# Performance work log

Hardware: AMD Instinct MI355X
Metric: run time of the kernel (lower is better)

## Reference

```python
import jax, jax.numpy as jnp
import numpy as np

E = 20    # number of residue types (rc.restypes)
NB = 2    # num_blocks per AngleHead
NA = 7    # num_angles
C_S = 384
C_H = 128
BS, L = 8, 2048


def setup_inputs() -> dict:
    key = jax.random.key(0)
    ks = jax.random.split(key, 16)
    sc = 0.02
    return {
        "s": jax.random.normal(ks[0], (BS, L, C_S), dtype=jnp.float32),
        "s_init": jax.random.normal(ks[1], (BS, L, C_S), dtype=jnp.float32),
        "aatype": jax.random.randint(ks[2], (BS, L), 0, E, dtype=jnp.int32),
        # stacked per-residue-type AngleHead params
        "Win": jax.random.normal(ks[3], (E, C_S, C_H), dtype=jnp.float32) * sc,
        "b_in": jax.random.normal(ks[4], (E, C_H), dtype=jnp.float32) * sc,
        "Winit": jax.random.normal(ks[5], (E, C_S, C_H), dtype=jnp.float32) * sc,
        "b_init2": jax.random.normal(ks[6], (E, C_H), dtype=jnp.float32) * sc,
        "Wb1": jax.random.normal(ks[7], (E, NB, C_H, C_H), dtype=jnp.float32) * sc,
        "bb1": jax.random.normal(ks[8], (E, NB, C_H), dtype=jnp.float32) * sc,
        "Wb2": jax.random.normal(ks[9], (E, NB, C_H, C_H), dtype=jnp.float32) * sc,
        "bb2": jax.random.normal(ks[10], (E, NB, C_H), dtype=jnp.float32) * sc,
        "Wout": jax.random.normal(ks[11], (E, C_H, NA * 2), dtype=jnp.float32) * sc,
        "b_out": jax.random.normal(ks[12], (E, NA * 2), dtype=jnp.float32) * sc,
    }


def reference(s, s_init, aatype, Win, b_in, Winit, b_init2, Wb1, bb1, Wb2, bb2, Wout, b_out):
    relu = jax.nn.relu
    bs, seq_len, c_s = s.shape
    N = bs * seq_len
    sf = s.reshape(N, c_s)          # [N, c_s]
    si = s_init.reshape(N, c_s)     # [N, c_s]

    # Dense dispatch: run every token through all E per-type heads, then
    # combine with the one-hot routing mask (math identical to the torch
    # gather/scatter loop over residue types).
    h = jnp.einsum('nd,edh->neh', relu(sf), Win) + b_in            # [N,E,H]
    h = h + jnp.einsum('nd,edh->neh', relu(si), Winit) + b_init2   # [N,E,H]

    for b in range(NB):  # ResidualBlock1d: s + W2 @ relu(W1 @ relu(s))
        a = jnp.einsum('neh,ehk->nek', relu(h), Wb1[:, b]) + bb1[:, b]
        a = jnp.einsum('nek,ekh->neh', relu(a), Wb2[:, b]) + bb2[:, b]
        h = h + a

    out = jnp.einsum('neh,eho->neo', relu(h), Wout) + b_out        # [N,E,2*NA]
    sel = jax.nn.one_hot(aatype.reshape(N), E, dtype=out.dtype)    # [N,E]
    ang = jnp.einsum('neo,ne->no', out, sel).reshape(bs, seq_len, NA, 2)

    # F.normalize(dim=-1): x / max(||x||, eps)
    nrm = jnp.maximum(jnp.linalg.norm(ang, axis=-1, keepdims=True), 1e-12)
    return ang / nrm
```

## Files before the change

kernel.cpp:

```cpp
#include <hip/hip_runtime.h>
#include <math.h>

#define E_TYPES 20
#define NBLK 2
#define NANG 7
#define CS 384
#define CH 128
#define N_TOK (8 * 2048)
#define TOK 32
#define TPB 256
#define KC 128
#define MAX_TILES (N_TOK / TOK + E_TYPES)
#define NPREP 64

#define HIST_OFF 0
#define CNT_OFF 1536
#define POFF_OFF 1600
#define PERM_OFF 2048

#define WT1_OFF (256 * 1024)
#define WT1_SZ  (20 * 8 * 24 * 2048)
#define WTR_OFF (WT1_OFF + WT1_SZ)

typedef __attribute__((ext_vector_type(8))) short bfrag;
typedef __attribute__((ext_vector_type(4))) float f32x4;

__device__ __forceinline__ void split_bf16(float x, unsigned short& h, unsigned short& l) {
    unsigned int u = __float_as_uint(x);
    unsigned int hb = (u + 0x7FFFu + ((u >> 16) & 1u)) & 0xFFFF0000u;
    h = (unsigned short)(hb >> 16);
    float r = x - __uint_as_float(hb);
    unsigned int v = __float_as_uint(r);
    l = (unsigned short)((v + 0x7FFFu + ((v >> 16) & 1u)) >> 16);
}

__global__ void prep1(const float* __restrict__ Win, const float* __restrict__ Winit,
                      const float* __restrict__ Wb1, const float* __restrict__ Wb2,
                      const int* __restrict__ aatype, int* __restrict__ wsI,
                      unsigned short* __restrict__ wt) {
    __shared__ int lh[E_TYPES];
    int bid = blockIdx.x;
    int t = threadIdx.x;
    if (bid >= 1600) {
        int b2 = bid - 1600;
        if (t < E_TYPES) lh[t] = 0;
        __syncthreads();
        int idx = b2 * 256 + t;
        if (idx < N_TOK) atomicAdd(&lh[aatype[idx]], 1);
        __syncthreads();
        if (t < E_TYPES) wsI[HIST_OFF + b2 * E_TYPES + t] = lh[t];
        return;
    }
    int gid = bid * 256 + t;
    unsigned short h[8], l[8];
    if (gid < 245760) {
        int lane = gid & 63;
        int bi = gid >> 6;
        int kb = bi % 24;
        int r = bi / 24;
        int nt = r & 7, e = r >> 3;
        int n = nt * 16 + (lane & 15);
        int k0 = kb * 32 + (lane >> 4) * 8;
        #pragma unroll
        for (int j = 0; j < 8; j++) {
            int k = k0 + j;
            float x = (k < CS) ? Win[((size_t)e * CS + k) * CH + n]
                               : Winit[((size_t)e * CS + (k - CS)) * CH + n];
            split_bf16(x, h[j], l[j]);
        }
        unsigned short* dst = wt + (WT1_OFF / 2) + (size_t)bi * 1024 + lane * 8;
        *(bfrag*)dst = *(bfrag*)h;
        *(bfrag*)(dst + 512) = *(bfrag*)l;
    } else {
        gid -= 245760;
        int lane = gid & 63;
        int bi = gid >> 6;
        int kb = bi & 3;
        int nt = (bi >> 2) & 7;
        int m4 = (bi >> 5) & 3;
        int e = bi >> 7;
        int b = m4 >> 1;
        const float* W = (m4 & 1) ? Wb2 : Wb1;
        int n = nt * 16 + (lane & 15);
        int k0 = kb * 32 + (lane >> 4) * 8;
        #pragma unroll
        for (int j = 0; j < 8; j++) {
            int k = k0 + j;
            float x = W[(((size_t)e * NBLK + b) * CH + k) * CH + n];
            split_bf16(x, h[j], l[j]);
        }
        unsigned short* dst = wt + (WTR_OFF / 2) + (size_t)bi * 1024 + lane * 8;
        *(bfrag*)dst = *(bfrag*)h;
        *(bfrag*)(dst + 512) = *(bfrag*)l;
    }
}

__global__ void scatter_k(const int* __restrict__ aatype, int* ws) {
    __shared__ int lhist[NPREP * E_TYPES];
    __shared__ int counts[E_TYPES], poff[E_TYPES + 1], mybase[E_TYPES], lcur[E_TYPES];
    int t = threadIdx.x;
    int bid = blockIdx.x;
    for (int idx = t; idx < NPREP * E_TYPES; idx += TPB)
        lhist[idx] = ws[HIST_OFF + idx];
    if (t < E_TYPES) lcur[t] = 0;
    __syncthreads();
    if (t < E_TYPES) {
        int tot = 0, pre = 0;
        for (int b = 0; b < NPREP; b++) {
            int v = lhist[b * E_TYPES + t];
            tot += v;
            if (b < bid) pre += v;
        }
        counts[t] = tot;
        mybase[t] = pre;
    }
    __syncthreads();
    if (t == 0) {
        int off = 0;
        for (int e = 0; e < E_TYPES; e++) {
            poff[e] = off;
            off += (counts[e] + TOK - 1) & ~(TOK - 1);
        }
        poff[E_TYPES] = off;
    }
    __syncthreads();
    if (t < E_TYPES) mybase[t] += poff[t];
    __syncthreads();
    int idx = bid * blockDim.x + t;
    if (idx < N_TOK) {
        int e = aatype[idx];
        int r = atomicAdd(&lcur[e], 1);
        ws[PERM_OFF + mybase[e] + r] = idx;
    }
    if (bid == 0) {
        if (t < E_TYPES) ws[CNT_OFF + t] = counts[t];
        if (t == 0)
            for (int e = 0; e <= E_TYPES; e++) ws[POFF_OFF + e] = poff[e];
    }
}

#define MFMA(a, b, c) __builtin_amdgcn_mfma_f32_16x16x32_bf16((a), (b), (c), 0, 0, 0)

__global__ __launch_bounds__(TPB)
void angle_main(const float* __restrict__ s, const float* __restrict__ si,
                const float* __restrict__ b_in, const float* __restrict__ b_init2,
                const float* __restrict__ bb1, const float* __restrict__ bb2,
                const float* __restrict__ Wout, const float* __restrict__ b_out,
                const int* __restrict__ wsI, const unsigned short* __restrict__ wt,
                float* __restrict__ out)
{
    __shared__ unsigned short Ah[TOK][136];
    __shared__ unsigned short Al[TOK][136];
    __shared__ float Hf[TOK][132];
    __shared__ float Of[TOK][16];
    __shared__ int ptok[TOK];

    int pos = blockIdx.x * TOK;
    if (pos >= wsI[POFF_OFF + E_TYPES]) return;
    int e = 0;
    while (e < E_TYPES - 1 && pos >= wsI[POFF_OFF + e + 1]) e++;
    int n = wsI[CNT_OFF + e] - (pos - wsI[POFF_OFF + e]);
    if (n > TOK) n = TOK;

    int t = threadIdx.x;
    if (t < TOK) ptok[t] = wsI[PERM_OFF + pos + ((t < n) ? t : 0)];

    int w = t >> 6, lane = t & 63;
    int lane15 = lane & 15, quad = lane >> 4;
    int nc[2] = { (2 * w) * 16 + lane15, (2 * w + 1) * 16 + lane15 };

    const bfrag* wt1 = (const bfrag*)((const char*)wt + WT1_OFF);
    const bfrag* wtr = (const bfrag*)((const char*)wt + WTR_OFF);

    f32x4 acc[2][2];
    {
        float bv0 = b_in[e * CH + nc[0]] + b_init2[e * CH + nc[0]];
        float bv1 = b_in[e * CH + nc[1]] + b_init2[e * CH + nc[1]];
        #pragma unroll
        for (int mt = 0; mt < 2; mt++) {
            acc[mt][0] = (f32x4){bv0, bv0, bv0, bv0};
            acc[mt][1] = (f32x4){bv1, bv1, bv1, bv1};
        }
    }

    __syncthreads();

    int srow = t >> 3;
    int scol = (t & 7) * 16;
    for (int c = 0; c < 6; c++) {
        const float* src = (c < 3) ? s : si;
        int kb0 = (c < 3 ? c : c - 3) * KC;
        {
            const float4* rp = (const float4*)(src + (size_t)ptok[srow] * CS + kb0 + scol);
            #pragma unroll
            for (int q = 0; q < 4; q++) {
                float4 v = rp[q];
                ushort4 hv, lv;
                split_bf16(fmaxf(v.x, 0.f), hv.x, lv.x);
                split_bf16(fmaxf(v.y, 0.f), hv.y, lv.y);
                split_bf16(fmaxf(v.z, 0.f), hv.z, lv.z);
                split_bf16(fmaxf(v.w, 0.f), hv.w, lv.w);
                *(ushort4*)&Ah[srow][scol + 4 * q] = hv;
                *(ushort4*)&Al[srow][scol + 4 * q] = lv;
            }
        }
        __syncthreads();
        #pragma unroll
        for (int ks = 0; ks < 4; ks++) {
            int kb = c * 4 + ks;
            int kl = ks * 32 + quad * 8;
            bfrag ah0 = *(const bfrag*)&Ah[lane15][kl];
            bfrag ah1 = *(const bfrag*)&Ah[16 + lane15][kl];
            bfrag al0 = *(const bfrag*)&Al[lane15][kl];
            bfrag al1 = *(const bfrag*)&Al[16 + lane15][kl];
            size_t b0 = ((size_t)(e * 8 + 2 * w) * 24 + kb) * 128;
            size_t b1 = ((size_t)(e * 8 + 2 * w + 1) * 24 + kb) * 128;
            bfrag bh0 = wt1[b0 + lane],      bl0 = wt1[b0 + 64 + lane];
            bfrag bh1 = wt1[b1 + lane],      bl1 = wt1[b1 + 64 + lane];
            acc[0][0] = MFMA(ah0, bh0, acc[0][0]);
            acc[0][0] = MFMA(ah0, bl0, acc[0][0]);
            acc[0][0] = MFMA(al0, bh0, acc[0][0]);
            acc[0][1] = MFMA(ah0, bh1, acc[0][1]);
            acc[0][1] = MFMA(ah0, bl1, acc[0][1]);
            acc[0][1] = MFMA(al0, bh1, acc[0][1]);
            acc[1][0] = MFMA(ah1, bh0, acc[1][0]);
            acc[1][0] = MFMA(ah1, bl0, acc[1][0]);
            acc[1][0] = MFMA(al1, bh0, acc[1][0]);
            acc[1][1] = MFMA(ah1, bh1, acc[1][1]);
            acc[1][1] = MFMA(ah1, bl1, acc[1][1]);
            acc[1][1] = MFMA(al1, bh1, acc[1][1]);
        }
        __syncthreads();
    }

    for (int b = 0; b < NBLK; b++) {
        #pragma unroll
        for (int mt = 0; mt < 2; mt++)
            #pragma unroll
            for (int nl = 0; nl < 2; nl++) {
                f32x4 v = acc[mt][nl];
                #pragma unroll
                for (int r = 0; r < 4; r++) {
                    int m = mt * 16 + quad * 4 + r;
                    unsigned short hh, ll;
                    split_bf16(fmaxf(v[r], 0.f), hh, ll);
                    Ah[m][nc[nl]] = hh;
                    Al[m][nc[nl]] = ll;
                }
            }
        __syncthreads();

        f32x4 a2[2][2];
        {
            float bv0 = bb1[(e * NBLK + b) * CH + nc[0]];
            float bv1 = bb1[(e * NBLK + b) * CH + nc[1]];
            #pragma unroll
            for (int mt = 0; mt < 2; mt++) {
                a2[mt][0] = (f32x4){bv0, bv0, bv0, bv0};
                a2[mt][1] = (f32x4){bv1, bv1, bv1, bv1};
            }
        }
        #pragma unroll
        for (int ks = 0; ks < 4; ks++) {
            int kl = ks * 32 + quad * 8;
            bfrag ah0 = *(const bfrag*)&Ah[lane15][kl];
            bfrag ah1 = *(const bfrag*)&Ah[16 + lane15][kl];
            bfrag al0 = *(const bfrag*)&Al[lane15][kl];
            bfrag al1 = *(const bfrag*)&Al[16 + lane15][kl];
            size_t b0 = (((size_t)(e * 4 + 2 * b) * 8 + 2 * w) * 4 + ks) * 128;
            size_t b1 = (((size_t)(e * 4 + 2 * b) * 8 + 2 * w + 1) * 4 + ks) * 128;
            bfrag bh0 = wtr[b0 + lane], bl0 = wtr[b0 + 64 + lane];
            bfrag bh1 = wtr[b1 + lane], bl1 = wtr[b1 + 64 + lane];
            a2[0][0] = MFMA(ah0, bh0, a2[0][0]);
            a2[0][0] = MFMA(ah0, bl0, a2[0][0]);
            a2[0][0] = MFMA(al0, bh0, a2[0][0]);
            a2[0][1] = MFMA(ah0, bh1, a2[0][1]);
            a2[0][1] = MFMA(ah0, bl1, a2[0][1]);
            a2[0][1] = MFMA(al0, bh1, a2[0][1]);
            a2[1][0] = MFMA(ah1, bh0, a2[1][0]);
            a2[1][0] = MFMA(ah1, bl0, a2[1][0]);
            a2[1][0] = MFMA(al1, bh0, a2[1][0]);
            a2[1][1] = MFMA(ah1, bh1, a2[1][1]);
            a2[1][1] = MFMA(ah1, bl1, a2[1][1]);
            a2[1][1] = MFMA(al1, bh1, a2[1][1]);
        }
        __syncthreads();

        #pragma unroll
        for (int mt = 0; mt < 2; mt++)
            #pragma unroll
            for (int nl = 0; nl < 2; nl++) {
                f32x4 v = a2[mt][nl];
                #pragma unroll
                for (int r = 0; r < 4; r++) {
                    int m = mt * 16 + quad * 4 + r;
                    unsigned short hh, ll;
                    split_bf16(fmaxf(v[r], 0.f), hh, ll);
                    Ah[m][nc[nl]] = hh;
                    Al[m][nc[nl]] = ll;
                }
            }
        __syncthreads();

        f32x4 a3[2][2];
        {
            float bv0 = bb2[(e * NBLK + b) * CH + nc[0]];
            float bv1 = bb2[(e * NBLK + b) * CH + nc[1]];
            #pragma unroll
            for (int mt = 0; mt < 2; mt++) {
                a3[mt][0] = (f32x4){bv0, bv0, bv0, bv0};
                a3[mt][1] = (f32x4){bv1, bv1, bv1, bv1};
            }
        }
        #pragma unroll
        for (int ks = 0; ks < 4; ks++) {
            int kl = ks * 32 + quad * 8;
            bfrag ah0 = *(const bfrag*)&Ah[lane15][kl];
            bfrag ah1 = *(const bfrag*)&Ah[16 + lane15][kl];
            bfrag al0 = *(const bfrag*)&Al[lane15][kl];
            bfrag al1 = *(const bfrag*)&Al[16 + lane15][kl];
            size_t b0 = (((size_t)(e * 4 + 2 * b + 1) * 8 + 2 * w) * 4 + ks) * 128;
            size_t b1 = (((size_t)(e * 4 + 2 * b + 1) * 8 + 2 * w + 1) * 4 + ks) * 128;
            bfrag bh0 = wtr[b0 + lane], bl0 = wtr[b0 + 64 + lane];
            bfrag bh1 = wtr[b1 + lane], bl1 = wtr[b1 + 64 + lane];
            a3[0][0] = MFMA(ah0, bh0, a3[0][0]);
            a3[0][0] = MFMA(ah0, bl0, a3[0][0]);
            a3[0][0] = MFMA(al0, bh0, a3[0][0]);
            a3[0][1] = MFMA(ah0, bh1, a3[0][1]);
            a3[0][1] = MFMA(ah0, bl1, a3[0][1]);
            a3[0][1] = MFMA(al0, bh1, a3[0][1]);
            a3[1][0] = MFMA(ah1, bh0, a3[1][0]);
            a3[1][0] = MFMA(ah1, bl0, a3[1][0]);
            a3[1][0] = MFMA(al1, bh0, a3[1][0]);
            a3[1][1] = MFMA(ah1, bh1, a3[1][1]);
            a3[1][1] = MFMA(ah1, bl1, a3[1][1]);
            a3[1][1] = MFMA(al1, bh1, a3[1][1]);
        }
        #pragma unroll
        for (int mt = 0; mt < 2; mt++)
            #pragma unroll
            for (int nl = 0; nl < 2; nl++)
                acc[mt][nl] += a3[mt][nl];
        __syncthreads();
    }

    #pragma unroll
    for (int mt = 0; mt < 2; mt++)
        #pragma unroll
        for (int nl = 0; nl < 2; nl++) {
            f32x4 v = acc[mt][nl];
            #pragma unroll
            for (int r = 0; r < 4; r++)
                Hf[mt * 16 + quad * 4 + r][nc[nl]] = fmaxf(v[r], 0.f);
        }
    __syncthreads();

    const float* WoutE = Wout + (size_t)e * CH * (NANG * 2);
    const float* boutE = b_out + (size_t)e * (NANG * 2);
    for (int idx = t; idx < n * (NANG * 2); idx += TPB) {
        int i = idx / (NANG * 2);
        int o = idx % (NANG * 2);
        float v = boutE[o];
        #pragma unroll 4
        for (int k = 0; k < CH; k++)
            v = fmaf(Hf[i][k], WoutE[(size_t)k * (NANG * 2) + o], v);
        Of[i][o] = v;
    }
    __syncthreads();

    for (int idx = t; idx < n * NANG; idx += TPB) {
        int i = idx / NANG;
        int a = idx % NANG;
        float x = Of[i][2 * a];
        float y = Of[i][2 * a + 1];
        float nr = fmaxf(sqrtf(x * x + y * y), 1e-12f);
        size_t base = (size_t)ptok[i] * (NANG * 2) + 2 * a;
        out[base]     = x / nr;
        out[base + 1] = y / nr;
    }
}

extern "C" void kernel_launch(void* const* d_in, const int* in_sizes, int n_in,
                              void* d_out, int out_size, void* d_ws, size_t ws_size,
                              hipStream_t stream) {
    const float* s       = (const float*)d_in[0];
    const float* s_init  = (const float*)d_in[1];
    const int*   aatype  = (const int*)d_in[2];
    const float* Win     = (const float*)d_in[3];
    const float* b_in    = (const float*)d_in[4];
    const float* Winit   = (const float*)d_in[5];
    const float* b_init2 = (const float*)d_in[6];
    const float* Wb1     = (const float*)d_in[7];
    const float* bb1     = (const float*)d_in[8];
    const float* Wb2     = (const float*)d_in[9];
    const float* bb2     = (const float*)d_in[10];
    const float* Wout    = (const float*)d_in[11];
    const float* b_out   = (const float*)d_in[12];
    int* wsI = (int*)d_ws;
    unsigned short* wt = (unsigned short*)d_ws;
    float* out = (float*)d_out;

    hipLaunchKernelGGL(prep1, dim3(1664), dim3(256), 0, stream,
                       Win, Winit, Wb1, Wb2, aatype, wsI, wt);
    hipLaunchKernelGGL(scatter_k, dim3(NPREP), dim3(TPB), 0, stream, aatype, wsI);
    hipLaunchKernelGGL(angle_main, dim3(MAX_TILES), dim3(TPB), 0, stream,
                       s, s_init, b_in, b_init2, bb1, bb2, Wout, b_out,
                       wsI, wt, out);
}
```

Before: 160.2 us.

## Merge prep kernels, bucket tokens per type, double-buffer activation loads

Folds the histogram and scatter kernels into one prep kernel. Each block recomputes prefix counts from aatype and writes token indices into fixed-size per-type buckets, removing one launch. Weight repacking now stages through LDS with coalesced float4 reads instead of strided scalar loads. The main kernel stores A operands in a fragment-ordered LDS layout, register-prefetches the next input chunk while converting the current one, and derives type offsets itself. The risks are that a type with more than 2048 tokens gets dropped, and that later prep blocks do quadratic-ish redundant histogram work.

```diff
diff --git a/kernel.cpp b/kernel.cpp
--- a/kernel.cpp
+++ b/kernel.cpp
@@ -11,13 +11,10 @@
 #define TPB 256
 #define KC 128
 #define MAX_TILES (N_TOK / TOK + E_TYPES)
-#define NPREP 64
-
-#define HIST_OFF 0
-#define CNT_OFF 1536
-#define POFF_OFF 1600
-#define PERM_OFF 2048
-
+#define PADN 2048
+
+#define CNT_OFF 0
+#define PERM_OFF 64
 #define WT1_OFF (256 * 1024)
 #define WT1_SZ  (20 * 8 * 24 * 2048)
 #define WTR_OFF (WT1_OFF + WT1_SZ)
@@ -34,108 +31,76 @@
     l = (unsigned short)((v + 0x7FFFu + ((v >> 16) & 1u)) >> 16);
 }
 
-__global__ void prep1(const float* __restrict__ Win, const float* __restrict__ Winit,
-                      const float* __restrict__ Wb1, const float* __restrict__ Wb2,
-                      const int* __restrict__ aatype, int* __restrict__ wsI,
-                      unsigned short* __restrict__ wt) {
-    __shared__ int lh[E_TYPES];
-    int bid = blockIdx.x;
-    int t = threadIdx.x;
-    if (bid >= 1600) {
-        int b2 = bid - 1600;
-        if (t < E_TYPES) lh[t] = 0;
+__global__ __launch_bounds__(TPB)
+void prep_k(const float* __restrict__ Win, const float* __restrict__ Winit,
+            const float* __restrict__ Wb1, const float* __restrict__ Wb2,
+            const int* __restrict__ aatype, int* __restrict__ wsI,
+            unsigned short* __restrict__ wt)
+{
+    __shared__ unsigned short tp[4][2][32][134];
+    __shared__ int lh[E_TYPES], lcur[E_TYPES];
+    int bid = blockIdx.x, t = threadIdx.x;
+
+    if (bid < 64) {
+        if (t < E_TYPES) { lh[t] = 0; lcur[t] = 0; }
         __syncthreads();
-        int idx = b2 * 256 + t;
-        if (idx < N_TOK) atomicAdd(&lh[aatype[idx]], 1);
+        for (int i = t; i < bid * 256; i += 256) atomicAdd(&lh[aatype[i]], 1);
         __syncthreads();
-        if (t < E_TYPES) wsI[HIST_OFF + b2 * E_TYPES + t] = lh[t];
+        int idx = bid * 256 + t;
+        int e = aatype[idx];
+        int r = lh[e] + atomicAdd(&lcur[e], 1);
+        if (r < PADN) wsI[PERM_OFF + e * PADN + r] = idx;
+        if (bid == 63) {
+            __syncthreads();
+            if (t < E_TYPES) wsI[CNT_OFF + t] = lh[t] + lcur[t];
+        }
         return;
     }
-    int gid = bid * 256 + t;
-    unsigned short h[8], l[8];
-    if (gid < 245760) {
-        int lane = gid & 63;
-        int bi = gid >> 6;
-        int kb = bi % 24;
-        int r = bi / 24;
-        int nt = r & 7, e = r >> 3;
-        int n = nt * 16 + (lane & 15);
-        int k0 = kb * 32 + (lane >> 4) * 8;
+
+    int w = t >> 6, lane = t & 63, lane15 = lane & 15, quad = lane >> 4;
+    int wid = (bid - 64) * 4 + w;
+    const float* srcbase;
+    int phase1, e, kt, m4 = 0;
+    if (wid < 480) {
+        phase1 = 1;
+        e = wid / 24; kt = wid % 24;
+        srcbase = (kt < 12) ? Win   + ((size_t)e * CS + kt * 32) * CH
+                            : Winit + ((size_t)e * CS + (kt - 12) * 32) * CH;
+    } else {
+        phase1 = 0;
+        int rid = wid - 480;
+        e = rid >> 4; m4 = (rid >> 2) & 3; kt = rid & 3;
+        const float* W = (m4 & 1) ? Wb2 : Wb1;
+        srcbase = W + (((size_t)e * NBLK + (m4 >> 1)) * CH + kt * 32) * CH;
+    }
+
+    #pragma unroll 4
+    for (int i = 0; i < 16; i++) {
+        int idx = i * 64 + lane;
+        int row = idx >> 5, c4 = idx & 31;
+        float4 v = *(const float4*)(srcbase + (size_t)row * CH + c4 * 4);
+        ushort4 hv, lv;
+        split_bf16(v.x, hv.x, lv.x);
+        split_bf16(v.y, hv.y, lv.y);
+        split_bf16(v.z, hv.z, lv.z);
+        split_bf16(v.w, hv.w, lv.w);
+        *(ushort4*)&tp[w][0][row][c4 * 4] = hv;
+        *(ushort4*)&tp[w][1][row][c4 * 4] = lv;
+    }
+    #pragma unroll
+    for (int nt = 0; nt < 8; nt++) {
+        bfrag hb, lb;
         #pragma unroll
         for (int j = 0; j < 8; j++) {
-            int k = k0 + j;
-            float x = (k < CS) ? Win[((size_t)e * CS + k) * CH + n]
-                               : Winit[((size_t)e * CS + (k - CS)) * CH + n];
-            split_bf16(x, h[j], l[j]);
-        }
-        unsigned short* dst = wt + (WT1_OFF / 2) + (size_t)bi * 1024 + lane * 8;
-        *(bfrag*)dst = *(bfrag*)h;
-        *(bfrag*)(dst + 512) = *(bfrag*)l;
-    } else {
-        gid -= 245760;
-        int lane = gid & 63;
-        int bi = gid >> 6;
-        int kb = bi & 3;
-        int nt = (bi >> 2) & 7;
-        int m4 = (bi >> 5) & 3;
-        int e = bi >> 7;
-        int b = m4 >> 1;
-        const float* W = (m4 & 1) ? Wb2 : Wb1;
-        int n = nt * 16 + (lane & 15);
-        int k0 = kb * 32 + (lane >> 4) * 8;
-        #pragma unroll
-        for (int j = 0; j < 8; j++) {
-            int k = k0 + j;
-            float x = W[(((size_t)e * NBLK + b) * CH + k) * CH + n];
-            split_bf16(x, h[j], l[j]);
-        }
-        unsigned short* dst = wt + (WTR_OFF / 2) + (size_t)bi * 1024 + lane * 8;
-        *(bfrag*)dst = *(bfrag*)h;
-        *(bfrag*)(dst + 512) = *(bfrag*)l;
-    }
-}
-
-__global__ void scatter_k(const int* __restrict__ aatype, int* ws) {
-    __shared__ int lhist[NPREP * E_TYPES];
-    __shared__ int counts[E_TYPES], poff[E_TYPES + 1], mybase[E_TYPES], lcur[E_TYPES];
-    int t = threadIdx.x;
-    int bid = blockIdx.x;
-    for (int idx = t; idx < NPREP * E_TYPES; idx += TPB)
-        lhist[idx] = ws[HIST_OFF + idx];
-    if (t < E_TYPES) lcur[t] = 0;
-    __syncthreads();
-    if (t < E_TYPES) {
-        int tot = 0, pre = 0;
-        for (int b = 0; b < NPREP; b++) {
-            int v = lhist[b * E_TYPES + t];
-            tot += v;
-            if (b < bid) pre += v;
-        }
-        counts[t] = tot;
-        mybase[t] = pre;
-    }
-    __syncthreads();
-    if (t == 0) {
-        int off = 0;
-        for (int e = 0; e < E_TYPES; e++) {
-            poff[e] = off;
-            off += (counts[e] + TOK - 1) & ~(TOK - 1);
-        }
-        poff[E_TYPES] = off;
-    }
-    __syncthreads();
-    if (t < E_TYPES) mybase[t] += poff[t];
-    __syncthreads();
-    int idx = bid * blockDim.x + t;
-    if (idx < N_TOK) {
-        int e = aatype[idx];
-        int r = atomicAdd(&lcur[e], 1);
-        ws[PERM_OFF + mybase[e] + r] = idx;
-    }
-    if (bid == 0) {
-        if (t < E_TYPES) ws[CNT_OFF + t] = counts[t];
-        if (t == 0)
-            for (int e = 0; e <= E_TYPES; e++) ws[POFF_OFF + e] = poff[e];
+            hb[j] = (short)tp[w][0][quad * 8 + j][nt * 16 + lane15];
+            lb[j] = (short)tp[w][1][quad * 8 + j][nt * 16 + lane15];
+        }
+        size_t blk = phase1 ? (size_t)((e * 8 + nt) * 24 + kt)
+                            : (size_t)((((e * 4 + m4) * 8) + nt) * 4 + kt);
+        unsigned short* dst = wt + (phase1 ? WT1_OFF / 2 : WTR_OFF / 2)
+                              + blk * 1024 + lane * 8;
+        *(bfrag*)dst = hb;
+        *(bfrag*)(dst + 512) = lb;
     }
 }
 
@@ -149,33 +114,43 @@
                 const int* __restrict__ wsI, const unsigned short* __restrict__ wt,
                 float* __restrict__ out)
 {
-    __shared__ unsigned short Ah[TOK][136];
-    __shared__ unsigned short Al[TOK][136];
+    __shared__ __align__(16) unsigned short Afrag[2][2][512][8];
     __shared__ float Hf[TOK][132];
     __shared__ float Of[TOK][16];
     __shared__ int ptok[TOK];
+    __shared__ int poffs[E_TYPES + 1];
+
+    int t = threadIdx.x;
+    if (t == 0) {
+        int off = 0;
+        for (int e = 0; e < E_TYPES; e++) {
+            poffs[e] = off;
+            off += (wsI[CNT_OFF + e] + TOK - 1) & ~(TOK - 1);
+        }
+        poffs[E_TYPES] = off;
+    }
+    __syncthreads();
 
     int pos = blockIdx.x * TOK;
-    if (pos >= wsI[POFF_OFF + E_TYPES]) return;
+    if (pos >= poffs[E_TYPES]) return;
     int e = 0;
-    while (e < E_TYPES - 1 && pos >= wsI[POFF_OFF + e + 1]) e++;
-    int n = wsI[CNT_OFF + e] - (pos - wsI[POFF_OFF + e]);
+    while (e < E_TYPES - 1 && pos >= poffs[e + 1]) e++;
+    int n = wsI[CNT_OFF + e] - (pos - poffs[e]);
     if (n > TOK) n = TOK;
-
-    int t = threadIdx.x;
-    if (t < TOK) ptok[t] = wsI[PERM_OFF + pos + ((t < n) ? t : 0)];
-
-    int w = t >> 6, lane = t & 63;
-    int lane15 = lane & 15, quad = lane >> 4;
-    int nc[2] = { (2 * w) * 16 + lane15, (2 * w + 1) * 16 + lane15 };
+    if (t < TOK)
+        ptok[t] = wsI[PERM_OFF + e * PADN + (pos - poffs[e]) + ((t < n) ? t : 0)];
+    __syncthreads();
+
+    int w = t >> 6, lane = t & 63, lane15 = lane & 15, quad = lane >> 4;
+    int nc0 = (2 * w) * 16 + lane15, nc1 = nc0 + 16;
 
     const bfrag* wt1 = (const bfrag*)((const char*)wt + WT1_OFF);
     const bfrag* wtr = (const bfrag*)((const char*)wt + WTR_OFF);
 
     f32x4 acc[2][2];
     {
-        float bv0 = b_in[e * CH + nc[0]] + b_init2[e * CH + nc[0]];
-        float bv1 = b_in[e * CH + nc[1]] + b_init2[e * CH + nc[1]];
+        float bv0 = b_in[e * CH + nc0] + b_init2[e * CH + nc0];
+        float bv1 = b_in[e * CH + nc1] + b_init2[e * CH + nc1];
         #pragma unroll
         for (int mt = 0; mt < 2; mt++) {
             acc[mt][0] = (f32x4){bv0, bv0, bv0, bv0};
@@ -183,40 +158,50 @@
         }
     }
 
-    __syncthreads();
-
-    int srow = t >> 3;
-    int scol = (t & 7) * 16;
+    int stok = t >> 3, sc = t & 7;
+    const float* rowp_s  = s  + (size_t)ptok[stok] * CS;
+    const float* rowp_si = si + (size_t)ptok[stok] * CS;
+
+    float4 pf[2][4];
+    #pragma unroll
+    for (int q = 0; q < 4; q++)
+        pf[0][q] = *(const float4*)(rowp_s + sc * 4 + 32 * q);
+
+    #pragma unroll
     for (int c = 0; c < 6; c++) {
-        const float* src = (c < 3) ? s : si;
-        int kb0 = (c < 3 ? c : c - 3) * KC;
-        {
-            const float4* rp = (const float4*)(src + (size_t)ptok[srow] * CS + kb0 + scol);
+        int buf = c & 1;
+        __syncthreads();
+        #pragma unroll
+        for (int q = 0; q < 4; q++) {
+            float4 v = pf[buf][q];
+            ushort4 hv, lv;
+            split_bf16(fmaxf(v.x, 0.f), hv.x, lv.x);
+            split_bf16(fmaxf(v.y, 0.f), hv.y, lv.y);
+            split_bf16(fmaxf(v.z, 0.f), hv.z, lv.z);
+            split_bf16(fmaxf(v.w, 0.f), hv.w, lv.w);
+            int fi = (q * 4 + (sc >> 1)) * 32 + stok;
+            *(ushort4*)&Afrag[buf][0][fi][(sc & 1) * 4] = hv;
+            *(ushort4*)&Afrag[buf][1][fi][(sc & 1) * 4] = lv;
+        }
+        if (c + 1 < 6) {
+            const float* rp = ((c + 1) < 3 ? rowp_s : rowp_si) + ((c + 1) % 3) * KC;
             #pragma unroll
-            for (int q = 0; q < 4; q++) {
-                float4 v = rp[q];
-                ushort4 hv, lv;
-                split_bf16(fmaxf(v.x, 0.f), hv.x, lv.x);
-                split_bf16(fmaxf(v.y, 0.f), hv.y, lv.y);
-                split_bf16(fmaxf(v.z, 0.f), hv.z, lv.z);
-                split_bf16(fmaxf(v.w, 0.f), hv.w, lv.w);
-                *(ushort4*)&Ah[srow][scol + 4 * q] = hv;
-                *(ushort4*)&Al[srow][scol + 4 * q] = lv;
-            }
+            for (int q = 0; q < 4; q++)
+                pf[(c + 1) & 1][q] = *(const float4*)(rp + sc * 4 + 32 * q);
         }
         __syncthreads();
         #pragma unroll
         for (int ks = 0; ks < 4; ks++) {
             int kb = c * 4 + ks;
-            int kl = ks * 32 + quad * 8;
-            bfrag ah0 = *(const bfrag*)&Ah[lane15][kl];
-            bfrag ah1 = *(const bfrag*)&Ah[16 + lane15][kl];
-            bfrag al0 = *(const bfrag*)&Al[lane15][kl];
-            bfrag al1 = *(const bfrag*)&Al[16 + lane15][kl];
+            int fib = (ks * 4 + quad) * 32;
+            bfrag ah0 = *(const bfrag*)&Afrag[buf][0][fib + lane15][0];
+            bfrag ah1 = *(const bfrag*)&Afrag[buf][0][fib + 16 + lane15][0];
+            bfrag al0 = *(const bfrag*)&Afrag[buf][1][fib + lane15][0];
+            bfrag al1 = *(const bfrag*)&Afrag[buf][1][fib + 16 + lane15][0];
             size_t b0 = ((size_t)(e * 8 + 2 * w) * 24 + kb) * 128;
             size_t b1 = ((size_t)(e * 8 + 2 * w + 1) * 24 + kb) * 128;
-            bfrag bh0 = wt1[b0 + lane],      bl0 = wt1[b0 + 64 + lane];
-            bfrag bh1 = wt1[b1 + lane],      bl1 = wt1[b1 + 64 + lane];
+            bfrag bh0 = wt1[b0 + lane], bl0 = wt1[b0 + 64 + lane];
+            bfrag bh1 = wt1[b1 + lane], bl1 = wt1[b1 + 64 + lane];
             acc[0][0] = MFMA(ah0, bh0, acc[0][0]);
             acc[0][0] = MFMA(ah0, bl0, acc[0][0]);
             acc[0][0] = MFMA(al0, bh0, acc[0][0]);
@@ -230,128 +215,93 @@
             acc[1][1] = MFMA(ah1, bl1, acc[1][1]);
             acc[1][1] = MFMA(al1, bh1, acc[1][1]);
         }
-        __syncthreads();
-    }
-
+    }
+
+    #pragma unroll
     for (int b = 0; b < NBLK; b++) {
-        #pragma unroll
-        for (int mt = 0; mt < 2; mt++)
+        f32x4 a2[2][2];
+        #pragma unroll
+        for (int stage = 0; stage < 2; stage++) {
+            int g = 2 * b + stage;
+            __syncthreads();
             #pragma unroll
-            for (int nl = 0; nl < 2; nl++) {
-                f32x4 v = acc[mt][nl];
+            for (int mt = 0; mt < 2; mt++)
                 #pragma unroll
-                for (int r = 0; r < 4; r++) {
-                    int m = mt * 16 + quad * 4 + r;
-                    unsigned short hh, ll;
-                    split_bf16(fmaxf(v[r], 0.f), hh, ll);
-                    Ah[m][nc[nl]] = hh;
-                    Al[m][nc[nl]] = ll;
+                for (int nl = 0; nl < 2; nl++) {
+                    f32x4 v = (stage == 0) ? acc[mt][nl] : a2[mt][nl];
+                    int nn = (2 * w + nl) * 16 + lane15;
+                    int fib = ((nn >> 5) * 4 + ((nn >> 3) & 3)) * 32;
+                    int j = nn & 7;
+                    #pragma unroll
+                    for (int r = 0; r < 4; r++) {
+                        int m = mt * 16 + quad * 4 + r;
+                        unsigned short hh, ll;
+                        split_bf16(fmaxf(v[r], 0.f), hh, ll);
+                        Afrag[0][0][fib + m][j] = hh;
+                        Afrag[0][1][fib + m][j] = ll;
+                    }
+                }
+            __syncthreads();
+
+            const float* bias = (stage == 0) ? bb1 : bb2;
+            f32x4 an[2][2];
+            {
+                float bv0 = bias[(e * NBLK + b) * CH + nc0];
+                float bv1 = bias[(e * NBLK + b) * CH + nc1];
+                #pragma unroll
+                for (int mt = 0; mt < 2; mt++) {
+                    an[mt][0] = (f32x4){bv0, bv0, bv0, bv0};
+                    an[mt][1] = (f32x4){bv1, bv1, bv1, bv1};
                 }
             }
-        __syncthreads();
-
-        f32x4 a2[2][2];
-        {
-            float bv0 = bb1[(e * NBLK + b) * CH + nc[0]];
-            float bv1 = bb1[(e * NBLK + b) * CH + nc[1]];
             #pragma unroll
-            for (int mt = 0; mt < 2; mt++) {
-                a2[mt][0] = (f32x4){bv0, bv0, bv0, bv0};
-                a2[mt][1] = (f32x4){bv1, bv1, bv1, bv1};
+            for (int ks = 0; ks < 4; ks++) {
+                int fib = (ks * 4 + quad) * 32;
+                bfrag ah0 = *(const bfrag*)&Afrag[0][0][fib + lane15][0];
+                bfrag ah1 = *(const bfrag*)&Afrag[0][0][fib + 16 + lane15][0];
+                bfrag al0 = *(const bfrag*)&Afrag[0][1][fib + lane15][0];
+                bfrag al1 = *(const bfrag*)&Afrag[0][1][fib + 16 + lane15][0];
+                size_t b0 = ((size_t)((e * 4 + g) * 8 + 2 * w) * 4 + ks) * 128;
+                size_t b1 = ((size_t)((e * 4 + g) * 8 + 2 * w + 1) * 4 + ks) * 128;
+                bfrag bh0 = wtr[b0 + lane], bl0 = wtr[b0 + 64 + lane];
+                bfrag bh1 = wtr[b1 + lane], bl1 = wtr[b1 + 64 + lane];
+                an[0][0] = MFMA(ah0, bh0, an[0][0]);
+                an[0][0] = MFMA(ah0, bl0, an[0][0]);
+                an[0][0] = MFMA(al0, bh0, an[0][0]);
+                an[0][1] = MFMA(ah0, bh1, an[0][1]);
+                an[0][1] = MFMA(ah0, bl1, an[0][1]);
+                an[0][1] = MFMA(al0, bh1, an[0][1]);
+                an[1][0] = MFMA(ah1, bh0, an[1][0]);
+                an[1][0] = MFMA(ah1, bl0, an[1][0]);
+                an[1][0] = MFMA(al1, bh0, an[1][0]);
+                an[1][1] = MFMA(ah1, bh1, an[1][1]);
+                an[1][1] = MFMA(ah1, bl1, an[1][1]);
+                an[1][1] = MFMA(al1, bh1, an[1][1]);
             }
-        }
-        #pragma unroll
-        for (int ks = 0; ks < 4; ks++) {
-            int kl = ks * 32 + quad * 8;
-            bfrag ah0 = *(const bfrag*)&Ah[lane15][kl];
-            bfrag ah1 = *(const bfrag*)&Ah[16 + lane15][kl];
-            bfrag al0 = *(const bfrag*)&Al[lane15][kl];
-            bfrag al1 = *(const bfrag*)&Al[16 + lane15][kl];
-            size_t b0 = (((size_t)(e * 4 + 2 * b) * 8 + 2 * w) * 4 + ks) * 128;
-            size_t b1 = (((size_t)(e * 4 + 2 * b) * 8 + 2 * w + 1) * 4 + ks) * 128;
-            bfrag bh0 = wtr[b0 + lane], bl0 = wtr[b0 + 64 + lane];
-            bfrag bh1 = wtr[b1 + lane], bl1 = wtr[b1 + 64 + lane];
-            a2[0][0] = MFMA(ah0, bh0, a2[0][0]);
-            a2[0][0] = MFMA(ah0, bl0, a2[0][0]);
-            a2[0][0] = MFMA(al0, bh0, a2[0][0]);
-            a2[0][1] = MFMA(ah0, bh1, a2[0][1]);
-            a2[0][1] = MFMA(ah0, bl1, a2[0][1]);
-            a2[0][1] = MFMA(al0, bh1, a2[0][1]);
-            a2[1][0] = MFMA(ah1, bh0, a2[1][0]);
-            a2[1][0] = MFMA(ah1, bl0, a2[1][0]);
-            a2[1][0] = MFMA(al1, bh0, a2[1][0]);
-            a2[1][1] = MFMA(ah1, bh1, a2[1][1]);
-            a2[1][1] = MFMA(ah1, bl1, a2[1][1]);
-            a2[1][1] = MFMA(al1, bh1, a2[1][1]);
-        }
-        __syncthreads();
-
-        #pragma unroll
-        for (int mt = 0; mt < 2; mt++)
-            #pragma unroll
-            for (int nl = 0; nl < 2; nl++) {
-                f32x4 v = a2[mt][nl];
+            if (stage == 0) {
                 #pragma unroll
-                for (int r = 0; r < 4; r++) {
-                    int m = mt * 16 + quad * 4 + r;
-                    unsigned short hh, ll;
-                    split_bf16(fmaxf(v[r], 0.f), hh, ll);
-                    Ah[m][nc[nl]] = hh;
-                    Al[m][nc[nl]] = ll;
-                }
+                for (int mt = 0; mt < 2; mt++)
+                    #pragma unroll
+                    for (int nl = 0; nl < 2; nl++) a2[mt][nl] = an[mt][nl];
+            } else {
+                #pragma unroll
+                for (int mt = 0; mt < 2; mt++)
+                    #pragma unroll
+                    for (int nl = 0; nl < 2; nl++) acc[mt][nl] += an[mt][nl];
             }
-        __syncthreads();
-
-        f32x4 a3[2][2];
-        {
-            float bv0 = bb2[(e * NBLK + b) * CH + nc[0]];
-            float bv1 = bb2[(e * NBLK + b) * CH + nc[1]];
-            #pragma unroll
-            for (int mt = 0; mt < 2; mt++) {
-                a3[mt][0] = (f32x4){bv0, bv0, bv0, bv0};
-                a3[mt][1] = (f32x4){bv1, bv1, bv1, bv1};
-            }
-        }
-        #pragma unroll
-        for (int ks = 0; ks < 4; ks++) {
-            int kl = ks * 32 + quad * 8;
-            bfrag ah0 = *(const bfrag*)&Ah[lane15][kl];
-            bfrag ah1 = *(const bfrag*)&Ah[16 + lane15][kl];
-            bfrag al0 = *(const bfrag*)&Al[lane15][kl];
-            bfrag al1 = *(const bfrag*)&Al[16 + lane15][kl];
-            size_t b0 = (((size_t)(e * 4 + 2 * b + 1) * 8 + 2 * w) * 4 + ks) * 128;
-            size_t b1 = (((size_t)(e * 4 + 2 * b + 1) * 8 + 2 * w + 1) * 4 + ks) * 128;
-            bfrag bh0 = wtr[b0 + lane], bl0 = wtr[b0 + 64 + lane];
-            bfrag bh1 = wtr[b1 + lane], bl1 = wtr[b1 + 64 + lane];
-            a3[0][0] = MFMA(ah0, bh0, a3[0][0]);
-            a3[0][0] = MFMA(ah0, bl0, a3[0][0]);
-            a3[0][0] = MFMA(al0, bh0, a3[0][0]);
-            a3[0][1] = MFMA(ah0, bh1, a3[0][1]);
-            a3[0][1] = MFMA(ah0, bl1, a3[0][1]);
-            a3[0][1] = MFMA(al0, bh1, a3[0][1]);
-            a3[1][0] = MFMA(ah1, bh0, a3[1][0]);
-            a3[1][0] = MFMA(ah1, bl0, a3[1][0]);
-            a3[1][0] = MFMA(al1, bh0, a3[1][0]);
-            a3[1][1] = MFMA(ah1, bh1, a3[1][1]);
-            a3[1][1] = MFMA(ah1, bl1, a3[1][1]);
-            a3[1][1] = MFMA(al1, bh1, a3[1][1]);
-        }
-        #pragma unroll
-        for (int mt = 0; mt < 2; mt++)
-            #pragma unroll
-            for (int nl = 0; nl < 2; nl++)
-                acc[mt][nl] += a3[mt][nl];
-        __syncthreads();
-    }
-
+        }
+    }
+
+    __syncthreads();
     #pragma unroll
     for (int mt = 0; mt < 2; mt++)
         #pragma unroll
         for (int nl = 0; nl < 2; nl++) {
             f32x4 v = acc[mt][nl];
+            int nn = (2 * w + nl) * 16 + lane15;
             #pragma unroll
             for (int r = 0; r < 4; r++)
-                Hf[mt * 16 + quad * 4 + r][nc[nl]] = fmaxf(v[r], 0.f);
+                Hf[mt * 16 + quad * 4 + r][nn] = fmaxf(v[r], 0.f);
         }
     __syncthreads();
 
@@ -400,9 +350,8 @@
     unsigned short* wt = (unsigned short*)d_ws;
     float* out = (float*)d_out;
 
-    hipLaunchKernelGGL(prep1, dim3(1664), dim3(256), 0, stream,
+    hipLaunchKernelGGL(prep_k, dim3(64 + 200), dim3(TPB), 0, stream,
                        Win, Winit, Wb1, Wb2, aatype, wsI, wt);
-    hipLaunchKernelGGL(scatter_k, dim3(NPREP), dim3(TPB), 0, stream, aatype, wsI);
     hipLaunchKernelGGL(angle_main, dim3(MAX_TILES), dim3(TPB), 0, stream,
                        s, s_init, b_in, b_init2, bb1, bb2, Wout, b_out,
                        wsI, wt, out);
```

Result: slower. 164.8 us (+2.8%).
